# Optimization experiments

Hardware: AMD Instinct MI355X
Metric: run time of the kernel (lower is better)

Reference implementation:

```python
import jax, jax.numpy as jnp
import numpy as np

B, N, D_MODEL = 16, 65536, 512
NBUCKETS = 11
BN_EPS = 1e-5
LN_EPS = 1e-5


def setup_inputs() -> dict:
    key = jax.random.key(0)
    ks = jax.random.split(key, 12)
    def w(k, shape, fan_in):
        return jax.random.normal(k, shape, jnp.float32) * (1.0 / np.sqrt(fan_in))
    return {
        "x": jax.random.normal(ks[0], (B, N, 3), jnp.float32),
        "w1": w(ks[1], (3, 64), 3),   "b1": jnp.zeros((64,), jnp.float32),
        "g1": jnp.ones((64,), jnp.float32),  "be1": jnp.zeros((64,), jnp.float32),
        "w2": w(ks[2], (64, 128), 64), "b2": jnp.zeros((128,), jnp.float32),
        "g2": jnp.ones((128,), jnp.float32), "be2": jnp.zeros((128,), jnp.float32),
        "w3": w(ks[3], (128, 256), 128), "b3": jnp.zeros((256,), jnp.float32),
        "g3": jnp.ones((256,), jnp.float32), "be3": jnp.zeros((256,), jnp.float32),
        "wp": w(ks[4], (518, D_MODEL), 518), "bp": jnp.zeros((D_MODEL,), jnp.float32),
        "g_ln": jnp.ones((D_MODEL,), jnp.float32), "b_ln": jnp.zeros((D_MODEL,), jnp.float32),
    }


def _bn(h, g, b):
    # BatchNorm1d in training mode: biased variance over the flattened batch axis
    m = jnp.mean(h, axis=0)
    v = jnp.mean((h - m) ** 2, axis=0)
    return (h - m) * jax.lax.rsqrt(v + BN_EPS) * g + b


def reference(x, w1, b1, g1, be1, w2, b2, g2, be2, w3, b3, g3, be3, wp, bp, g_ln, b_ln):
    Bb, Nn, _ = x.shape
    x_flat = x.reshape(Bb * Nn, 3)
    h = jax.nn.relu(_bn(x_flat @ w1 + b1, g1, be1))
    h = jax.nn.relu(_bn(h @ w2 + b2, g2, be2))
    h = jax.nn.relu(_bn(h @ w3 + b3, g3, be3))
    feat = h.reshape(Bb, Nn, 256)

    # y-bucket histogram means of (x, z) coordinates, vectorized via segment_sum
    y = x[:, :, 1]
    y_min = jnp.min(y, axis=1, keepdims=True)
    y_max = jnp.max(y, axis=1, keepdims=True)
    y_norm = (y - y_min) / (y_max - y_min + 1e-6)
    buckets = jnp.clip((y_norm * 10).astype(jnp.int32), 0, NBUCKETS - 1)  # (B,N) in [0,10]
    seg = (jnp.arange(Bb, dtype=jnp.int32)[:, None] * NBUCKETS + buckets).reshape(-1)
    nseg = Bb * NBUCKETS
    sx = jax.ops.segment_sum(x[:, :, 0].reshape(-1), seg, num_segments=nseg)
    sz = jax.ops.segment_sum(x[:, :, 2].reshape(-1), seg, num_segments=nseg)
    cnt = jax.ops.segment_sum(jnp.ones((Bb * Nn,), jnp.float32), seg, num_segments=nseg)
    denom = jnp.maximum(cnt, 1.0)
    cx = (sx / denom).reshape(Bb, NBUCKETS)
    cz = (sz / denom).reshape(Bb, NBUCKETS)
    x_centers = jnp.take_along_axis(cx, buckets, axis=1)  # (B,N)
    z_centers = jnp.take_along_axis(cz, buckets, axis=1)

    dx = x[:, :, 0] - x_centers
    dz = x[:, :, 2] - z_centers
    theta = jnp.arctan2(dz, dx)
    r = jnp.sqrt(dx ** 2 + dz ** 2)
    spatial = jnp.stack([jnp.sin(theta), jnp.cos(theta), r], axis=-1)  # (B,N,3)

    feat = jnp.concatenate([feat, spatial], axis=-1)  # (B,N,259)
    feat_max = jnp.max(feat, axis=1)
    feat_avg = jnp.mean(feat, axis=1)
    feat_cat = jnp.concatenate([feat_max, feat_avg], axis=1)  # (B,518)

    out = feat_cat @ wp + bp
    mu = jnp.mean(out, axis=-1, keepdims=True)
    var = jnp.mean((out - mu) ** 2, axis=-1, keepdims=True)
    return (out - mu) * jax.lax.rsqrt(var + LN_EPS) * g_ln + b_ln
```

## Files before the change

### kernel.cpp

```cpp
#include <hip/hip_runtime.h>
#include <stdint.h>

#define B_    16
#define N_    65536
#define NPTS  (B_*N_)
#define NBK   11
#define NFEAT 259
#define NF    ((float)NPTS)

typedef float f32x4 __attribute__((ext_vector_type(4)));
typedef short s16x8 __attribute__((ext_vector_type(8)));

enum {
  OFF_YMINF = 16,
  OFF_YMAXF = 32,
  OFF_A1    = 64,
  OFF_C1    = 128,
  OFF_A2    = 192,
  OFF_C2    = 320,
  OFF_CX    = 448,
  OFF_CZ    = 624,
  OFF_A3    = 800,
  OFF_C3    = 1056,
  OFF_PSTR  = 16384,
  OFF_PBKT  = 24576,
  OFF_PH2   = 49152,
  OFF_PH3   = 180224,
  OFF_PPOOL = 442368,
  OFF_PSPA  = 704512
};

__device__ __forceinline__ float wave_sum(float v){
  #pragma unroll
  for (int m=32;m>=1;m>>=1) v += __shfl_xor(v,m,64);
  return v;
}
__device__ __forceinline__ float wave_max(float v){
  #pragma unroll
  for (int m=32;m>=1;m>>=1) v = fmaxf(v,__shfl_xor(v,m,64));
  return v;
}
__device__ __forceinline__ float wave_min(float v){
  #pragma unroll
  for (int m=32;m>=1;m>>=1) v = fminf(v,__shfl_xor(v,m,64));
  return v;
}
__device__ __forceinline__ unsigned short bf16_bits(float f){
  unsigned u=__float_as_uint(f);
  u += 0x7FFFu + ((u>>16)&1u);
  return (unsigned short)(u>>16);
}

__global__ __launch_bounds__(256) void k_stream0(const float* __restrict__ x,
                                                 float* __restrict__ ws){
  __shared__ float red[4][12];
  const int t=threadIdx.x, l=t&63, w=t>>6;
  const int bid=blockIdx.x;
  const float4* xv=(const float4*)(x + (size_t)bid*2048*3);
  float s0=0,s1=0,s2=0,q00=0,q01=0,q02=0,q11=0,q12=0,q22=0;
  float ymn=3.4e38f, ymx=-3.4e38f;
  #pragma unroll
  for (int i=0;i<2;i++){
    const int vi=(i*256+t)*3;
    const float4 a=xv[vi], b4=xv[vi+1], c=xv[vi+2];
    float X[4]={a.x,a.w,b4.z,c.y};
    float Y[4]={a.y,b4.x,b4.w,c.z};
    float Z[4]={a.z,b4.y,c.x,c.w};
    #pragma unroll
    for (int p=0;p<4;p++){
      s0+=X[p]; s1+=Y[p]; s2+=Z[p];
      q00=fmaf(X[p],X[p],q00); q01=fmaf(X[p],Y[p],q01); q02=fmaf(X[p],Z[p],q02);
      q11=fmaf(Y[p],Y[p],q11); q12=fmaf(Y[p],Z[p],q12); q22=fmaf(Z[p],Z[p],q22);
      ymn=fminf(ymn,Y[p]); ymx=fmaxf(ymx,Y[p]);
    }
  }
  s0=wave_sum(s0); s1=wave_sum(s1); s2=wave_sum(s2);
  q00=wave_sum(q00); q01=wave_sum(q01); q02=wave_sum(q02);
  q11=wave_sum(q11); q12=wave_sum(q12); q22=wave_sum(q22);
  ymn=wave_min(ymn); ymx=wave_max(ymx);
  if (l==0){
    red[w][0]=s0; red[w][1]=s1; red[w][2]=s2;
    red[w][3]=q00; red[w][4]=q01; red[w][5]=q02;
    red[w][6]=q11; red[w][7]=q12; red[w][8]=q22;
    red[w][9]=ymn; red[w][10]=ymx;
  }
  __syncthreads();
  if (t<11){
    const float v0=red[0][t],v1=red[1][t],v2=red[2][t],v3=red[3][t];
    float r;
    if (t==9)       r=fminf(fminf(v0,v1),fminf(v2,v3));
    else if (t==10) r=fmaxf(fmaxf(v0,v1),fmaxf(v2,v3));
    else            r=v0+v1+v2+v3;
    ws[OFF_PSTR+bid*16+t]=r;
  }
}

__global__ void k_finA(const float* __restrict__ w1, const float* __restrict__ b1,
                       const float* __restrict__ gm, const float* __restrict__ bt,
                       float* __restrict__ ws){
  __shared__ float sums[9];
  const int t=threadIdx.x;
  if (t<9){
    float s=0.f;
    #pragma unroll 8
    for (int blk=0;blk<512;blk++) s+=ws[OFF_PSTR+blk*16+t];
    sums[t]=s;
  }
  if (t>=32&&t<48){
    const int b=t-32; float m=3.4e38f;
    #pragma unroll 8
    for (int blk=0;blk<32;blk++) m=fminf(m,ws[OFF_PSTR+(b*32+blk)*16+9]);
    ws[OFF_YMINF+b]=m;
  }
  if (t>=48&&t<64){
    const int b=t-48; float m=-3.4e38f;
    #pragma unroll 8
    for (int blk=0;blk<32;blk++) m=fmaxf(m,ws[OFF_PSTR+(b*32+blk)*16+10]);
    ws[OFF_YMAXF+b]=m;
  }
  __syncthreads();
  if (t<64){
    const float i_n=1.f/NF;
    const float w0=w1[t], wa=w1[64+t], wb=w1[128+t];
    const float ms=(w0*sums[0]+wa*sums[1]+wb*sums[2])*i_n;
    const float es=(w0*w0*sums[3]+wa*wa*sums[6]+wb*wb*sums[8]
                   +2.f*(w0*wa*sums[4]+w0*wb*sums[5]+wa*wb*sums[7]))*i_n;
    const float var=es-ms*ms;
    const float a=gm[t]/sqrtf(var+1e-5f);
    ws[OFF_A1+t]=a; ws[OFF_C1+t]=bt[t]-(ms+b1[t])*a;
  }
}

__global__ __launch_bounds__(256) void k_bucket(const float* __restrict__ x,
                                                float* __restrict__ ws){
  __shared__ float red[4][12];
  const int t=threadIdx.x, l=t&63, w=t>>6;
  const int bid=blockIdx.x, b=bid>>5;
  const float ymn=ws[OFF_YMINF+b], ymx=ws[OFF_YMAXF+b];
  const float4* xv=(const float4*)(x + (size_t)bid*2048*3);
  float sxl[NBK], szl[NBK], cntl[NBK];
  #pragma unroll
  for (int k=0;k<NBK;k++){ sxl[k]=0.f; szl[k]=0.f; cntl[k]=0.f; }
  #pragma unroll
  for (int i=0;i<2;i++){
    const int vi=(i*256+t)*3;
    const float4 a=xv[vi], b4=xv[vi+1], c=xv[vi+2];
    float X[4]={a.x,a.w,b4.z,c.y};
    float Y[4]={a.y,b4.x,b4.w,c.z};
    float Z[4]={a.z,b4.y,c.x,c.w};
    #pragma unroll
    for (int p=0;p<4;p++){
      const float yn=(Y[p]-ymn)/(ymx-ymn+1e-6f);
      int bk=(int)(yn*10.f); bk = bk<0?0:(bk>10?10:bk);
      #pragma unroll
      for (int k=0;k<NBK;k++){
        const bool m=(bk==k);
        sxl[k]+= m?X[p]:0.f; szl[k]+= m?Z[p]:0.f; cntl[k]+= m?1.f:0.f;
      }
    }
  }
  #pragma unroll
  for (int k=0;k<NBK;k++){
    const float s=wave_sum(sxl[k]);
    if (l==0) red[w][k]=s;
  }
  __syncthreads();
  if (t<NBK) ws[OFF_PBKT+bid*36+t]=red[0][t]+red[1][t]+red[2][t]+red[3][t];
  __syncthreads();
  #pragma unroll
  for (int k=0;k<NBK;k++){
    const float z=wave_sum(szl[k]);
    if (l==0) red[w][k]=z;
  }
  __syncthreads();
  if (t<NBK) ws[OFF_PBKT+bid*36+11+t]=red[0][t]+red[1][t]+red[2][t]+red[3][t];
  __syncthreads();
  #pragma unroll
  for (int k=0;k<NBK;k++){
    const float c=wave_sum(cntl[k]);
    if (l==0) red[w][k]=c;
  }
  __syncthreads();
  if (t<NBK) ws[OFF_PBKT+bid*36+22+t]=red[0][t]+red[1][t]+red[2][t]+red[3][t];
}

__global__ void k_finB(const float* __restrict__ gm, const float* __restrict__ bt,
                       float* __restrict__ ws){
  __shared__ float acc[256];
  const int t=threadIdx.x;
  {
    const int col=t&127, part=t>>7;
    float s=0.f;
    #pragma unroll 8
    for (int blk=0;blk<512;blk++) s+=ws[OFF_PH2+blk*256+part*128+col];
    acc[t]=s;
  }
  __syncthreads();
  if (t<128){
    const float i_n=1.f/NF;
    const float m=acc[t]*i_n;
    const float v=acc[128+t]*i_n-m*m;
    const float a=gm[t]/sqrtf(v+1e-5f);
    ws[OFF_A2+t]=a; ws[OFF_C2+t]=bt[t]-m*a;
  }
  if (t<176){
    const int b=t/NBK, k=t-b*NBK;
    float sx=0.f, sz=0.f, cn=0.f;
    #pragma unroll 8
    for (int blk=0;blk<32;blk++){
      const int p=OFF_PBKT+(b*32+blk)*36;
      sx+=ws[p+k]; sz+=ws[p+11+k]; cn+=ws[p+22+k];
    }
    const float d=fmaxf(cn,1.f);
    ws[OFF_CX+t]=sx/d; ws[OFF_CZ+t]=sz/d;
  }
}

__global__ void k_finC(const float* __restrict__ gm, const float* __restrict__ bt,
                       float* __restrict__ ws){
  __shared__ float acc[512];
  const int t=threadIdx.x;
  {
    const int col=t&255, part=t>>8;
    float s=0.f;
    #pragma unroll 8
    for (int blk=0;blk<512;blk++) s+=ws[OFF_PH3+blk*512+part*256+col];
    acc[t]=s;
  }
  __syncthreads();
  if (t<256){
    const float i_n=1.f/NF;
    const float m=acc[t]*i_n;
    const float v=acc[256+t]*i_n-m*m;
    const float a=gm[t]/sqrtf(v+1e-5f);
    ws[OFF_A3+t]=a; ws[OFF_C3+t]=bt[t]-m*a;
  }
}

__global__ __launch_bounds__(256) void k_spatial(const float* __restrict__ x,
                                                 float* __restrict__ ws){
  __shared__ float red[4][8];
  const int t=threadIdx.x, l=t&63, w=t>>6;
  const int bid=blockIdx.x, b=bid>>5;
  const float ymn=ws[OFF_YMINF+b], ymx=ws[OFF_YMAXF+b];
  const float4* xv=(const float4*)(x + (size_t)bid*2048*3);
  float mx[3]={-3.4e38f,-3.4e38f,-3.4e38f}, sm[3]={0.f,0.f,0.f};
  #pragma unroll
  for (int i=0;i<2;i++){
    const int vi=(i*256+t)*3;
    const float4 a=xv[vi], b4=xv[vi+1], c=xv[vi+2];
    float X[4]={a.x,a.w,b4.z,c.y};
    float Y[4]={a.y,b4.x,b4.w,c.z};
    float Z[4]={a.z,b4.y,c.x,c.w};
    #pragma unroll
    for (int p=0;p<4;p++){
      const float yn=(Y[p]-ymn)/(ymx-ymn+1e-6f);
      int bk=(int)(yn*10.f); bk = bk<0?0:(bk>10?10:bk);
      const float dx=X[p]-ws[OFF_CX+b*NBK+bk];
      const float dz=Z[p]-ws[OFF_CZ+b*NBK+bk];
      const float r=sqrtf(fmaf(dx,dx,dz*dz));
      const float sn=(r>0.f)?(dz/r):0.f;
      const float cs=(r>0.f)?(dx/r):1.f;
      mx[0]=fmaxf(mx[0],sn); sm[0]+=sn;
      mx[1]=fmaxf(mx[1],cs); sm[1]+=cs;
      mx[2]=fmaxf(mx[2],r);  sm[2]+=r;
    }
  }
  #pragma unroll
  for (int q=0;q<3;q++){
    const float m=wave_max(mx[q]);
    const float s=wave_sum(sm[q]);
    if (l==0){ red[w][q]=m; red[w][4+q]=s; }
  }
  __syncthreads();
  if (t<3)        ws[OFF_PSPA+bid*8+t]  =fmaxf(fmaxf(red[0][t],red[1][t]),fmaxf(red[2][t],red[3][t]));
  else if (t>=4&&t<7){
    const int q=t-4;
    ws[OFF_PSPA+bid*8+4+q]=red[0][4+q]+red[1][4+q]+red[2][4+q]+red[3][4+q];
  }
}

template<int MODE>
__global__ __launch_bounds__(512,2) void k_mlp(
    const float* __restrict__ x,
    const float* __restrict__ w1, const float* __restrict__ b1,
    const float* __restrict__ w2, const float* __restrict__ b2,
    const float* __restrict__ w3, const float* __restrict__ b3,
    float* __restrict__ ws)
{
  __shared__ short g1t[128*72];
  __shared__ short g2t[128*136];
  const int t=threadIdx.x, w=t>>6, l=t&63, lg=l>>4, lr=l&15;
  const int bid=blockIdx.x, b=bid>>5, chunk=bid&31;
  char* g1c=(char*)g1t; char* g2c=(char*)g2t;

  const int fg=l&7, pj=(l>>3)&7;
  const float* a1=ws+OFF_A1; const float* c1=ws+OFF_C1;
  float w1f[3][8], b1f[8];
  #pragma unroll
  for (int i=0;i<8;i++){
    const int f=8*fg+i; const float a=a1[f];
    #pragma unroll
    for (int q=0;q<3;q++) w1f[q][i]=w1[q*64+f]*a;
    b1f[i]=b1[f]*a+c1[f];
  }

  s16x8 w2f[2]; float b2v[4];
  {
    const int col2=16*w+lr;
    const float sc2=(MODE==0)?1.f:ws[OFF_A2+col2];
    #pragma unroll
    for (int kt=0;kt<2;kt++)
      #pragma unroll
      for (int i=0;i<8;i++)
        w2f[kt][i]=(short)bf16_bits(w2[(kt*32+8*lg+i)*128+col2]*sc2);
    #pragma unroll
    for (int r=0;r<4;r++){
      const int f2=16*w+4*lg+r;
      b2v[r]=(MODE==0)? b2[f2] : (ws[OFF_A2+f2]*b2[f2]+ws[OFF_C2+f2]);
    }
  }

  s16x8 w3f[2][4]; float b3v[2][4];
  if (MODE!=0){
    #pragma unroll
    for (int ft=0;ft<2;ft++){
      const int col3=(2*w+ft)*16+lr;
      const float sc3=(MODE==1)?1.f:ws[OFF_A3+col3];
      #pragma unroll
      for (int kt=0;kt<4;kt++)
        #pragma unroll
        for (int i=0;i<8;i++)
          w3f[ft][kt][i]=(short)bf16_bits(w3[(kt*32+8*lg+i)*256+col3]*sc3);
      #pragma unroll
      for (int r=0;r<4;r++){
        const int f3=(2*w+ft)*16+4*lg+r;
        b3v[ft][r]=(MODE==1)? b3[f3] : (ws[OFF_A3+f3]*b3[f3]+ws[OFF_C3+f3]);
      }
    }
  }

  float aS[2][4], aQ[2][4];
  #pragma unroll
  for (int ft=0;ft<2;ft++)
    #pragma unroll
    for (int r=0;r<4;r++){ aS[ft][r]=(MODE==2)?-3.4e38f:0.f; aQ[ft][r]=0.f; }

  const int base=b*N_+chunk*2048;

  #pragma unroll 1
  for (int it=0; it<16; ++it){
    const int tb=base+it*128;
    #pragma unroll
    for (int s=0;s<2;s++){
      const int pt=16*w+2*pj+s;
      const float x0=x[(tb+pt)*3+0], x1v=x[(tb+pt)*3+1], x2=x[(tb+pt)*3+2];
      unsigned pk[4];
      #pragma unroll
      for (int i=0;i<4;i++){
        float v0=b1f[2*i], v1=b1f[2*i+1];
        v0=fmaf(x0,w1f[0][2*i],v0);  v1=fmaf(x0,w1f[0][2*i+1],v1);
        v0=fmaf(x1v,w1f[1][2*i],v0); v1=fmaf(x1v,w1f[1][2*i+1],v1);
        v0=fmaf(x2,w1f[2][2*i],v0);  v1=fmaf(x2,w1f[2][2*i+1],v1);
        pk[i]=(unsigned)bf16_bits(fmaxf(v0,0.f))|((unsigned)bf16_bits(fmaxf(v1,0.f))<<16);
      }
      *(int4*)(g1c + pt*144 + fg*16) = make_int4(pk[0],pk[1],pk[2],pk[3]);
    }
    __syncthreads();
    #pragma unroll 2
    for (int ptile=0;ptile<8;ptile++){
      const int row=ptile*16+lr;
      const s16x8 bf0=*(const s16x8*)(g1c + row*144 + lg*16);
      const s16x8 bf1=*(const s16x8*)(g1c + row*144 + 64 + lg*16);
      f32x4 acc={0.f,0.f,0.f,0.f};
      acc=__builtin_amdgcn_mfma_f32_16x16x32_bf16(w2f[0],bf0,acc,0,0,0);
      acc=__builtin_amdgcn_mfma_f32_16x16x32_bf16(w2f[1],bf1,acc,0,0,0);
      if (MODE==0){
        #pragma unroll
        for (int r=0;r<4;r++){ const float h=acc[r]+b2v[r]; aS[0][r]+=h; aQ[0][r]+=h*h; }
      } else {
        const float g0=fmaxf(acc[0]+b2v[0],0.f), g1v=fmaxf(acc[1]+b2v[1],0.f);
        const float g2v=fmaxf(acc[2]+b2v[2],0.f), g3v=fmaxf(acc[3]+b2v[3],0.f);
        const unsigned lo=(unsigned)bf16_bits(g0)|((unsigned)bf16_bits(g1v)<<16);
        const unsigned hi=(unsigned)bf16_bits(g2v)|((unsigned)bf16_bits(g3v)<<16);
        *(uint2*)(g2c + row*272 + w*32 + lg*8) = make_uint2(lo,hi);
      }
    }
    __syncthreads();
    if (MODE!=0){
      #pragma unroll 1
      for (int ptile=0;ptile<8;ptile++){
        const int row=ptile*16+lr;
        s16x8 bf0=*(const s16x8*)(g2c + row*272 + lg*16);
        s16x8 bf1=*(const s16x8*)(g2c + row*272 + 64 + lg*16);
        f32x4 a0={0.f,0.f,0.f,0.f}, a1v={0.f,0.f,0.f,0.f};
        a0 =__builtin_amdgcn_mfma_f32_16x16x32_bf16(w3f[0][0],bf0,a0 ,0,0,0);
        a1v=__builtin_amdgcn_mfma_f32_16x16x32_bf16(w3f[1][0],bf0,a1v,0,0,0);
        a0 =__builtin_amdgcn_mfma_f32_16x16x32_bf16(w3f[0][1],bf1,a0 ,0,0,0);
        a1v=__builtin_amdgcn_mfma_f32_16x16x32_bf16(w3f[1][1],bf1,a1v,0,0,0);
        bf0=*(const s16x8*)(g2c + row*272 + 128 + lg*16);
        bf1=*(const s16x8*)(g2c + row*272 + 192 + lg*16);
        a0 =__builtin_amdgcn_mfma_f32_16x16x32_bf16(w3f[0][2],bf0,a0 ,0,0,0);
        a1v=__builtin_amdgcn_mfma_f32_16x16x32_bf16(w3f[1][2],bf0,a1v,0,0,0);
        a0 =__builtin_amdgcn_mfma_f32_16x16x32_bf16(w3f[0][3],bf1,a0 ,0,0,0);
        a1v=__builtin_amdgcn_mfma_f32_16x16x32_bf16(w3f[1][3],bf1,a1v,0,0,0);
        #pragma unroll
        for (int r=0;r<4;r++){
          if (MODE==1){
            const float h0=a0[r] +b3v[0][r]; aS[0][r]+=h0; aQ[0][r]+=h0*h0;
            const float h1=a1v[r]+b3v[1][r]; aS[1][r]+=h1; aQ[1][r]+=h1*h1;
          } else {
            const float g0=fmaxf(a0[r] +b3v[0][r],0.f);
            const float g1v=fmaxf(a1v[r]+b3v[1][r],0.f);
            aS[0][r]=fmaxf(aS[0][r],g0); aQ[0][r]+=g0;
            aS[1][r]=fmaxf(aS[1][r],g1v); aQ[1][r]+=g1v;
          }
        }
      }
    }
  }

  if (MODE==0){
    #pragma unroll
    for (int r=0;r<4;r++){
      float s=aS[0][r], q=aQ[0][r];
      #pragma unroll
      for (int m=1;m<16;m<<=1){ s+=__shfl_xor(s,m); q+=__shfl_xor(q,m); }
      if (lr==0){
        const int f2=16*w+4*lg+r;
        ws[OFF_PH2+bid*256+f2]    =s;
        ws[OFF_PH2+bid*256+128+f2]=q;
      }
    }
  } else if (MODE==1){
    #pragma unroll
    for (int ft=0;ft<2;ft++)
      #pragma unroll
      for (int r=0;r<4;r++){
        float s=aS[ft][r], q=aQ[ft][r];
        #pragma unroll
        for (int m=1;m<16;m<<=1){ s+=__shfl_xor(s,m); q+=__shfl_xor(q,m); }
        if (lr==0){
          const int f3=(2*w+ft)*16+4*lg+r;
          ws[OFF_PH3+bid*512+f3]    =s;
          ws[OFF_PH3+bid*512+256+f3]=q;
        }
      }
  } else {
    #pragma unroll
    for (int ft=0;ft<2;ft++)
      #pragma unroll
      for (int r=0;r<4;r++){
        float mxv=aS[ft][r], s=aQ[ft][r];
        #pragma unroll
        for (int m=1;m<16;m<<=1){ mxv=fmaxf(mxv,__shfl_xor(mxv,m)); s+=__shfl_xor(s,m); }
        if (lr==0){
          const int f3=(2*w+ft)*16+4*lg+r;
          ws[OFF_PPOOL+bid*512+f3]    =mxv;
          ws[OFF_PPOOL+bid*512+256+f3]=s;
        }
      }
  }
}

__global__ __launch_bounds__(256) void k_final(
    const float* __restrict__ wp, const float* __restrict__ bp,
    const float* __restrict__ gln, const float* __restrict__ bln,
    float* __restrict__ out, const float* __restrict__ ws)
{
  __shared__ float feat[518];
  __shared__ float red[256];
  const int b=blockIdx.x, t=threadIdx.x;
  {
    float fm=-3.4e38f, fs=0.f;
    #pragma unroll 4
    for (int blk=0;blk<32;blk++){
      const int p=OFF_PPOOL+(b*32+blk)*512;
      fm=fmaxf(fm,ws[p+t]);
      fs+=ws[p+256+t];
    }
    feat[t]=fm; feat[NFEAT+t]=fs*(1.f/65536.f);
  }
  if (t<3){
    float fm=-3.4e38f, fs=0.f;
    #pragma unroll 4
    for (int blk=0;blk<32;blk++){
      const int p=OFF_PSPA+(b*32+blk)*8;
      fm=fmaxf(fm,ws[p+t]);
      fs+=ws[p+4+t];
    }
    feat[256+t]=fm; feat[NFEAT+256+t]=fs*(1.f/65536.f);
  }
  __syncthreads();
  float o0=bp[t], o1=bp[t+256];
  #pragma unroll 4
  for (int i=0;i<518;i++){
    const float f=feat[i];
    o0=fmaf(f, wp[i*512+t],     o0);
    o1=fmaf(f, wp[i*512+t+256], o1);
  }
  red[t]=o0+o1; __syncthreads();
  for (int s=128;s>0;s>>=1){ if (t<s) red[t]+=red[t+s]; __syncthreads(); }
  const float mu=red[0]*(1.f/512.f);
  __syncthreads();
  const float d0=o0-mu, d1=o1-mu;
  red[t]=d0*d0+d1*d1; __syncthreads();
  for (int s=128;s>0;s>>=1){ if (t<s) red[t]+=red[t+s]; __syncthreads(); }
  const float var=red[0]*(1.f/512.f);
  const float rs=1.f/sqrtf(var+1e-5f);
  out[b*512+t]     = d0*rs*gln[t]    +bln[t];
  out[b*512+t+256] = d1*rs*gln[t+256]+bln[t+256];
}

extern "C" void kernel_launch(void* const* d_in, const int* in_sizes, int n_in,
                              void* d_out, int out_size, void* d_ws, size_t ws_size,
                              hipStream_t stream)
{
  const float* x  =(const float*)d_in[0];
  const float* w1 =(const float*)d_in[1];
  const float* b1 =(const float*)d_in[2];
  const float* gm1=(const float*)d_in[3];
  const float* be1=(const float*)d_in[4];
  const float* w2 =(const float*)d_in[5];
  const float* b2 =(const float*)d_in[6];
  const float* gm2=(const float*)d_in[7];
  const float* be2=(const float*)d_in[8];
  const float* w3 =(const float*)d_in[9];
  const float* b3 =(const float*)d_in[10];
  const float* gm3=(const float*)d_in[11];
  const float* be3=(const float*)d_in[12];
  const float* wp =(const float*)d_in[13];
  const float* bp =(const float*)d_in[14];
  const float* gln=(const float*)d_in[15];
  const float* bln=(const float*)d_in[16];
  float* ws=(float*)d_ws;
  float* out=(float*)d_out;

  k_stream0<<<dim3(512),dim3(256),0,stream>>>(x,ws);
  k_finA   <<<dim3(1),  dim3(256),0,stream>>>(w1,b1,gm1,be1,ws);
  k_bucket <<<dim3(512),dim3(256),0,stream>>>(x,ws);
  k_mlp<0> <<<dim3(512),dim3(512),0,stream>>>(x,w1,b1,w2,b2,w3,b3,ws);
  k_finB   <<<dim3(1),  dim3(256),0,stream>>>(gm2,be2,ws);
  k_spatial<<<dim3(512),dim3(256),0,stream>>>(x,ws);
  k_mlp<1> <<<dim3(512),dim3(512),0,stream>>>(x,w1,b1,w2,b2,w3,b3,ws);
  k_finC   <<<dim3(1),  dim3(512),0,stream>>>(gm3,be3,ws);
  k_mlp<2> <<<dim3(512),dim3(512),0,stream>>>(x,w1,b1,w2,b2,w3,b3,ws);
  k_final  <<<dim3(16), dim3(256),0,stream>>>(wp,bp,gln,bln,out,ws);
}
```

Measured before the change: 440.1 us.

## Retile MLP waves into point-group by feature-group to reuse LDS B-fragments

Each wave now handles half the point tiles (64 rows) and a larger feature group: 2 layer-2 column tiles and 4 layer-3 column tiles, instead of all 128 rows for 1 or 2 column tiles. Every B-fragment read from shared memory then feeds more MFMAs, which cuts LDS read traffic per MFMA. The cost is more weight-fragment and accumulator registers, so launch bounds drop to one block per CU. Per-block partial outputs double, and the finalize kernels and workspace offsets are enlarged to match.

```diff
diff --git a/kernel.cpp b/kernel.cpp
--- a/kernel.cpp
+++ b/kernel.cpp
@@ -25,9 +25,9 @@
   OFF_PSTR  = 16384,
   OFF_PBKT  = 24576,
   OFF_PH2   = 49152,
-  OFF_PH3   = 180224,
-  OFF_PPOOL = 442368,
-  OFF_PSPA  = 704512
+  OFF_PH3   = 311296,
+  OFF_PPOOL = 835584,
+  OFF_PSPA  = 1359872
 };
 
 __device__ __forceinline__ float wave_sum(float v){
@@ -192,7 +192,7 @@
     const int col=t&127, part=t>>7;
     float s=0.f;
     #pragma unroll 8
-    for (int blk=0;blk<512;blk++) s+=ws[OFF_PH2+blk*256+part*128+col];
+    for (int blk=0;blk<1024;blk++) s+=ws[OFF_PH2+blk*256+part*128+col];
     acc[t]=s;
   }
   __syncthreads();
@@ -224,7 +224,7 @@
     const int col=t&255, part=t>>8;
     float s=0.f;
     #pragma unroll 8
-    for (int blk=0;blk<512;blk++) s+=ws[OFF_PH3+blk*512+part*256+col];
+    for (int blk=0;blk<1024;blk++) s+=ws[OFF_PH3+blk*512+part*256+col];
     acc[t]=s;
   }
   __syncthreads();
@@ -281,7 +281,7 @@
 }
 
 template<int MODE>
-__global__ __launch_bounds__(512,2) void k_mlp(
+__global__ __launch_bounds__(512,1) void k_mlp(
     const float* __restrict__ x,
     const float* __restrict__ w1, const float* __restrict__ b1,
     const float* __restrict__ w2, const float* __restrict__ b2,
@@ -292,6 +292,7 @@
   __shared__ short g2t[128*136];
   const int t=threadIdx.x, w=t>>6, l=t&63, lg=l>>4, lr=l&15;
   const int bid=blockIdx.x, b=bid>>5, chunk=bid&31;
+  const int ptg=w&1, fgrp=w>>1;
   char* g1c=(char*)g1t; char* g2c=(char*)g2t;
 
   const int fg=l&7, pj=(l>>3)&7;
@@ -305,46 +306,47 @@
     b1f[i]=b1[f]*a+c1[f];
   }
 
-  s16x8 w2f[2]; float b2v[4];
-  {
-    const int col2=16*w+lr;
+  s16x8 w2f[2][2]; float b2v[2][4];
+  #pragma unroll
+  for (int j=0;j<2;j++){
+    const int col2=(2*fgrp+j)*16+lr;
     const float sc2=(MODE==0)?1.f:ws[OFF_A2+col2];
     #pragma unroll
     for (int kt=0;kt<2;kt++)
       #pragma unroll
       for (int i=0;i<8;i++)
-        w2f[kt][i]=(short)bf16_bits(w2[(kt*32+8*lg+i)*128+col2]*sc2);
+        w2f[j][kt][i]=(short)bf16_bits(w2[(kt*32+8*lg+i)*128+col2]*sc2);
     #pragma unroll
     for (int r=0;r<4;r++){
-      const int f2=16*w+4*lg+r;
-      b2v[r]=(MODE==0)? b2[f2] : (ws[OFF_A2+f2]*b2[f2]+ws[OFF_C2+f2]);
-    }
-  }
-
-  s16x8 w3f[2][4]; float b3v[2][4];
+      const int f2=(2*fgrp+j)*16+4*lg+r;
+      b2v[j][r]=(MODE==0)? b2[f2] : (ws[OFF_A2+f2]*b2[f2]+ws[OFF_C2+f2]);
+    }
+  }
+
+  s16x8 w3f[4][4]; float b3v[4][4];
   if (MODE!=0){
     #pragma unroll
-    for (int ft=0;ft<2;ft++){
-      const int col3=(2*w+ft)*16+lr;
+    for (int j=0;j<4;j++){
+      const int col3=(4*fgrp+j)*16+lr;
       const float sc3=(MODE==1)?1.f:ws[OFF_A3+col3];
       #pragma unroll
       for (int kt=0;kt<4;kt++)
         #pragma unroll
         for (int i=0;i<8;i++)
-          w3f[ft][kt][i]=(short)bf16_bits(w3[(kt*32+8*lg+i)*256+col3]*sc3);
+          w3f[j][kt][i]=(short)bf16_bits(w3[(kt*32+8*lg+i)*256+col3]*sc3);
       #pragma unroll
       for (int r=0;r<4;r++){
-        const int f3=(2*w+ft)*16+4*lg+r;
-        b3v[ft][r]=(MODE==1)? b3[f3] : (ws[OFF_A3+f3]*b3[f3]+ws[OFF_C3+f3]);
-      }
-    }
-  }
-
-  float aS[2][4], aQ[2][4];
-  #pragma unroll
-  for (int ft=0;ft<2;ft++)
-    #pragma unroll
-    for (int r=0;r<4;r++){ aS[ft][r]=(MODE==2)?-3.4e38f:0.f; aQ[ft][r]=0.f; }
+        const int f3=(4*fgrp+j)*16+4*lg+r;
+        b3v[j][r]=(MODE==1)? b3[f3] : (ws[OFF_A3+f3]*b3[f3]+ws[OFF_C3+f3]);
+      }
+    }
+  }
+
+  float aS[4][4], aQ[4][4];
+  #pragma unroll
+  for (int j=0;j<4;j++)
+    #pragma unroll
+    for (int r=0;r<4;r++){ aS[j][r]=(MODE==2)?-3.4e38f:0.f; aQ[j][r]=0.f; }
 
   const int base=b*N_+chunk*2048;
 
@@ -367,97 +369,99 @@
       *(int4*)(g1c + pt*144 + fg*16) = make_int4(pk[0],pk[1],pk[2],pk[3]);
     }
     __syncthreads();
-    #pragma unroll 2
-    for (int ptile=0;ptile<8;ptile++){
-      const int row=ptile*16+lr;
+    #pragma unroll
+    for (int pt=0;pt<4;pt++){
+      const int row=ptg*64+pt*16+lr;
       const s16x8 bf0=*(const s16x8*)(g1c + row*144 + lg*16);
       const s16x8 bf1=*(const s16x8*)(g1c + row*144 + 64 + lg*16);
-      f32x4 acc={0.f,0.f,0.f,0.f};
-      acc=__builtin_amdgcn_mfma_f32_16x16x32_bf16(w2f[0],bf0,acc,0,0,0);
-      acc=__builtin_amdgcn_mfma_f32_16x16x32_bf16(w2f[1],bf1,acc,0,0,0);
-      if (MODE==0){
-        #pragma unroll
-        for (int r=0;r<4;r++){ const float h=acc[r]+b2v[r]; aS[0][r]+=h; aQ[0][r]+=h*h; }
-      } else {
-        const float g0=fmaxf(acc[0]+b2v[0],0.f), g1v=fmaxf(acc[1]+b2v[1],0.f);
-        const float g2v=fmaxf(acc[2]+b2v[2],0.f), g3v=fmaxf(acc[3]+b2v[3],0.f);
-        const unsigned lo=(unsigned)bf16_bits(g0)|((unsigned)bf16_bits(g1v)<<16);
-        const unsigned hi=(unsigned)bf16_bits(g2v)|((unsigned)bf16_bits(g3v)<<16);
-        *(uint2*)(g2c + row*272 + w*32 + lg*8) = make_uint2(lo,hi);
+      #pragma unroll
+      for (int j=0;j<2;j++){
+        f32x4 acc={0.f,0.f,0.f,0.f};
+        acc=__builtin_amdgcn_mfma_f32_16x16x32_bf16(w2f[j][0],bf0,acc,0,0,0);
+        acc=__builtin_amdgcn_mfma_f32_16x16x32_bf16(w2f[j][1],bf1,acc,0,0,0);
+        if (MODE==0){
+          #pragma unroll
+          for (int r=0;r<4;r++){ const float h=acc[r]+b2v[j][r]; aS[j][r]+=h; aQ[j][r]+=h*h; }
+        } else {
+          const float g0=fmaxf(acc[0]+b2v[j][0],0.f), g1v=fmaxf(acc[1]+b2v[j][1],0.f);
+          const float g2v=fmaxf(acc[2]+b2v[j][2],0.f), g3v=fmaxf(acc[3]+b2v[j][3],0.f);
+          const unsigned lo=(unsigned)bf16_bits(g0)|((unsigned)bf16_bits(g1v)<<16);
+          const unsigned hi=(unsigned)bf16_bits(g2v)|((unsigned)bf16_bits(g3v)<<16);
+          *(uint2*)(g2c + row*272 + fgrp*64 + j*32 + lg*8) = make_uint2(lo,hi);
+        }
       }
     }
     __syncthreads();
     if (MODE!=0){
       #pragma unroll 1
-      for (int ptile=0;ptile<8;ptile++){
-        const int row=ptile*16+lr;
-        s16x8 bf0=*(const s16x8*)(g2c + row*272 + lg*16);
-        s16x8 bf1=*(const s16x8*)(g2c + row*272 + 64 + lg*16);
-        f32x4 a0={0.f,0.f,0.f,0.f}, a1v={0.f,0.f,0.f,0.f};
-        a0 =__builtin_amdgcn_mfma_f32_16x16x32_bf16(w3f[0][0],bf0,a0 ,0,0,0);
-        a1v=__builtin_amdgcn_mfma_f32_16x16x32_bf16(w3f[1][0],bf0,a1v,0,0,0);
-        a0 =__builtin_amdgcn_mfma_f32_16x16x32_bf16(w3f[0][1],bf1,a0 ,0,0,0);
-        a1v=__builtin_amdgcn_mfma_f32_16x16x32_bf16(w3f[1][1],bf1,a1v,0,0,0);
-        bf0=*(const s16x8*)(g2c + row*272 + 128 + lg*16);
-        bf1=*(const s16x8*)(g2c + row*272 + 192 + lg*16);
-        a0 =__builtin_amdgcn_mfma_f32_16x16x32_bf16(w3f[0][2],bf0,a0 ,0,0,0);
-        a1v=__builtin_amdgcn_mfma_f32_16x16x32_bf16(w3f[1][2],bf0,a1v,0,0,0);
-        a0 =__builtin_amdgcn_mfma_f32_16x16x32_bf16(w3f[0][3],bf1,a0 ,0,0,0);
-        a1v=__builtin_amdgcn_mfma_f32_16x16x32_bf16(w3f[1][3],bf1,a1v,0,0,0);
+      for (int pt=0;pt<4;pt++){
+        const int row=ptg*64+pt*16+lr;
+        const s16x8 bf0=*(const s16x8*)(g2c + row*272 + lg*16);
+        const s16x8 bf1=*(const s16x8*)(g2c + row*272 + 64 + lg*16);
+        const s16x8 bf2=*(const s16x8*)(g2c + row*272 + 128 + lg*16);
+        const s16x8 bf3=*(const s16x8*)(g2c + row*272 + 192 + lg*16);
         #pragma unroll
-        for (int r=0;r<4;r++){
-          if (MODE==1){
-            const float h0=a0[r] +b3v[0][r]; aS[0][r]+=h0; aQ[0][r]+=h0*h0;
-            const float h1=a1v[r]+b3v[1][r]; aS[1][r]+=h1; aQ[1][r]+=h1*h1;
-          } else {
-            const float g0=fmaxf(a0[r] +b3v[0][r],0.f);
-            const float g1v=fmaxf(a1v[r]+b3v[1][r],0.f);
-            aS[0][r]=fmaxf(aS[0][r],g0); aQ[0][r]+=g0;
-            aS[1][r]=fmaxf(aS[1][r],g1v); aQ[1][r]+=g1v;
+        for (int j=0;j<4;j++){
+          f32x4 a3={0.f,0.f,0.f,0.f};
+          a3=__builtin_amdgcn_mfma_f32_16x16x32_bf16(w3f[j][0],bf0,a3,0,0,0);
+          a3=__builtin_amdgcn_mfma_f32_16x16x32_bf16(w3f[j][1],bf1,a3,0,0,0);
+          a3=__builtin_amdgcn_mfma_f32_16x16x32_bf16(w3f[j][2],bf2,a3,0,0,0);
+          a3=__builtin_amdgcn_mfma_f32_16x16x32_bf16(w3f[j][3],bf3,a3,0,0,0);
+          #pragma unroll
+          for (int r=0;r<4;r++){
+            if (MODE==1){
+              const float h=a3[r]+b3v[j][r]; aS[j][r]+=h; aQ[j][r]+=h*h;
+            } else {
+              const float g=fmaxf(a3[r]+b3v[j][r],0.f);
+              aS[j][r]=fmaxf(aS[j][r],g); aQ[j][r]+=g;
+            }
           }
         }
       }
     }
   }
 
+  const int bid2=bid*2+ptg;
   if (MODE==0){
     #pragma unroll
-    for (int r=0;r<4;r++){
-      float s=aS[0][r], q=aQ[0][r];
-      #pragma unroll
-      for (int m=1;m<16;m<<=1){ s+=__shfl_xor(s,m); q+=__shfl_xor(q,m); }
-      if (lr==0){
-        const int f2=16*w+4*lg+r;
-        ws[OFF_PH2+bid*256+f2]    =s;
-        ws[OFF_PH2+bid*256+128+f2]=q;
-      }
-    }
-  } else if (MODE==1){
-    #pragma unroll
-    for (int ft=0;ft<2;ft++)
+    for (int j=0;j<2;j++)
       #pragma unroll
       for (int r=0;r<4;r++){
-        float s=aS[ft][r], q=aQ[ft][r];
+        float s=aS[j][r], q=aQ[j][r];
         #pragma unroll
         for (int m=1;m<16;m<<=1){ s+=__shfl_xor(s,m); q+=__shfl_xor(q,m); }
         if (lr==0){
-          const int f3=(2*w+ft)*16+4*lg+r;
-          ws[OFF_PH3+bid*512+f3]    =s;
-          ws[OFF_PH3+bid*512+256+f3]=q;
+          const int f2=(2*fgrp+j)*16+4*lg+r;
+          ws[OFF_PH2+bid2*256+f2]    =s;
+          ws[OFF_PH2+bid2*256+128+f2]=q;
         }
       }
+  } else if (MODE==1){
+    #pragma unroll
+    for (int j=0;j<4;j++)
+      #pragma unroll
+      for (int r=0;r<4;r++){
+        float s=aS[j][r], q=aQ[j][r];
+        #pragma unroll
+        for (int m=1;m<16;m<<=1){ s+=__shfl_xor(s,m); q+=__shfl_xor(q,m); }
+        if (lr==0){
+          const int f3=(4*fgrp+j)*16+4*lg+r;
+          ws[OFF_PH3+bid2*512+f3]    =s;
+          ws[OFF_PH3+bid2*512+256+f3]=q;
+        }
+      }
   } else {
     #pragma unroll
-    for (int ft=0;ft<2;ft++)
+    for (int j=0;j<4;j++)
       #pragma unroll
       for (int r=0;r<4;r++){
-        float mxv=aS[ft][r], s=aQ[ft][r];
+        float mxv=aS[j][r], s=aQ[j][r];
         #pragma unroll
         for (int m=1;m<16;m<<=1){ mxv=fmaxf(mxv,__shfl_xor(mxv,m)); s+=__shfl_xor(s,m); }
         if (lr==0){
-          const int f3=(2*w+ft)*16+4*lg+r;
-          ws[OFF_PPOOL+bid*512+f3]    =mxv;
-          ws[OFF_PPOOL+bid*512+256+f3]=s;
+          const int f3=(4*fgrp+j)*16+4*lg+r;
+          ws[OFF_PPOOL+bid2*512+f3]    =mxv;
+          ws[OFF_PPOOL+bid2*512+256+f3]=s;
         }
       }
   }
@@ -474,8 +478,8 @@
   {
     float fm=-3.4e38f, fs=0.f;
     #pragma unroll 4
-    for (int blk=0;blk<32;blk++){
-      const int p=OFF_PPOOL+(b*32+blk)*512;
+    for (int blk=0;blk<64;blk++){
+      const int p=OFF_PPOOL+(b*64+blk)*512;
       fm=fmaxf(fm,ws[p+t]);
       fs+=ws[p+256+t];
     }
```

New measurement: 508.6 us. +15.6%, slower.
